# Kernel optimization log

Hardware: AMD Instinct MI355X
Metric: run time of the kernel (lower is better)

## Reference

```python
import jax, jax.numpy as jnp
import numpy as np

D = 256          # feature_dim
H = 4            # num_heads (hard-coded in AdaAttentionalPropagation)
HD = D // H      # per-head dim = 64
L = 6            # number of layers
B, N, M = 2, 2048, 2048
NAMES = ("self", "cross", "self", "cross", "self", "cross")
POOLS = (1, 1, 2, 2, 2, 2)
EPS = 1e-5


def conv1x1(W, b, x):
    # Conv1d kernel_size=1 == pointwise linear over channels: x [B, Cin, N] -> [B, Cout, N]
    return jnp.einsum('oi,bin->bon', W, x) + b[None, :, None]


def inst_norm(x):
    # InstanceNorm1d(affine=False): normalize over spatial dim per (batch, channel)
    mu = jnp.mean(x, axis=-1, keepdims=True)
    var = jnp.var(x, axis=-1, keepdims=True)
    return (x - mu) * jax.lax.rsqrt(var + EPS)


def attn_prop(params, x, source, mask):
    # One AdaAttentionalPropagation layer. x [B,D,Nq], source [B,D,Nk], mask [B,Nq,Nk]
    Wq, bq, Wk, bk, Wv, bv, Wm, bm, W1, b1, W2, b2 = params
    b = x.shape[0]
    q = conv1x1(Wq, bq, x).reshape(b, HD, H, -1)       # [B, hd, H, Nq]
    k = conv1x1(Wk, bk, source).reshape(b, HD, H, -1)  # [B, hd, H, Nk]
    v = conv1x1(Wv, bv, source).reshape(b, HD, H, -1)
    scores = jnp.einsum('bdhn,bdhm->bhnm', q, k) / np.sqrt(HD).astype(np.float32)
    scores = scores * mask[:, None]                     # multiplicative pruned mask
    prob = jax.nn.softmax(scores, axis=-1)              # [B, H, Nq, Nk]
    att = jnp.einsum('bhnm,bdhm->bdhn', prob, v).reshape(b, D, -1)
    message = conv1x1(Wm, bm, att)                      # merge
    y = jnp.concatenate([x, message], axis=1)           # [B, 2D, Nq]
    h = jax.nn.relu(inst_norm(conv1x1(W1, b1, y)))      # MLP_IN hidden
    delta = conv1x1(W2, b2, h)                          # [B, D, Nq]
    return delta, jnp.mean(prob, axis=1)                # prob averaged over heads


def prune(conn, prob, pool, k_cur):
    # update_connections_by_pooling_size: keep top (k_cur // pool) entries per row
    if prob is None or pool == 1:
        return conn, k_cur
    k_new = k_cur // pool
    vals, idxs = jax.lax.top_k(prob, k_new)             # over last axis
    b, n, _ = conn.shape
    new = jnp.zeros_like(conn).at[
        jnp.arange(b)[:, None, None], jnp.arange(n)[None, :, None], idxs
    ].set(jnp.where(vals > 0, 1.0, 0.0).astype(conn.dtype))
    return jax.lax.stop_gradient(new), k_new


def setup_inputs() -> dict:
    key = jax.random.key(0)
    ks = jax.random.split(key, 16)
    s1 = 1.0 / np.sqrt(D)
    s2 = 1.0 / np.sqrt(2 * D)
    return {
        "desc0": jax.random.normal(ks[0], (B, D, N), dtype=jnp.float32),
        "desc1": jax.random.normal(ks[1], (B, D, M), dtype=jnp.float32),
        "Wq": jax.random.normal(ks[2], (L, D, D), dtype=jnp.float32) * s1,
        "bq": jax.random.normal(ks[3], (L, D), dtype=jnp.float32) * 0.01,
        "Wk": jax.random.normal(ks[4], (L, D, D), dtype=jnp.float32) * s1,
        "bk": jax.random.normal(ks[5], (L, D), dtype=jnp.float32) * 0.01,
        "Wv": jax.random.normal(ks[6], (L, D, D), dtype=jnp.float32) * s1,
        "bv": jax.random.normal(ks[7], (L, D), dtype=jnp.float32) * 0.01,
        "Wm": jax.random.normal(ks[8], (L, D, D), dtype=jnp.float32) * s1,
        "bm": jax.random.normal(ks[9], (L, D), dtype=jnp.float32) * 0.01,
        "W1": jax.random.normal(ks[10], (L, 2 * D, 2 * D), dtype=jnp.float32) * s2,
        "b1": jax.random.normal(ks[11], (L, 2 * D), dtype=jnp.float32) * 0.01,
        "W2": jax.random.normal(ks[12], (L, D, 2 * D), dtype=jnp.float32) * s2,
        "b2": jnp.zeros((L, D), dtype=jnp.float32),  # nn.init.constant_(mlp[-1].bias, 0)
    }


def reference(desc0, desc1, Wq, bq, Wk, bk, Wv, bv, Wm, bm, W1, b1, W2, b2):
    b = desc0.shape[0]
    n, m = desc0.shape[2], desc1.shape[2]
    masks = {
        '00': jnp.ones((b, n, n), jnp.float32), '01': jnp.ones((b, n, m), jnp.float32),
        '11': jnp.ones((b, m, m), jnp.float32), '10': jnp.ones((b, m, n), jnp.float32),
    }
    probs = {'00': None, '01': None, '11': None, '10': None}
    kcnt = {'00': n, '01': m, '11': m, '10': n}
    for i in range(L):
        params = (Wq[i], bq[i], Wk[i], bk[i], Wv[i], bv[i],
                  Wm[i], bm[i], W1[i], b1[i], W2[i], b2[i])
        pool = POOLS[i]
        if NAMES[i] == 'cross':
            masks['01'], kcnt['01'] = prune(masks['01'], probs['01'], pool, kcnt['01'])
            delta0, probs['01'] = attn_prop(params, desc0, desc1, masks['01'])
            masks['10'], kcnt['10'] = prune(masks['10'], probs['10'], pool, kcnt['10'])
            delta1, probs['10'] = attn_prop(params, desc1, desc0, masks['10'])
        else:
            masks['00'], kcnt['00'] = prune(masks['00'], probs['00'], pool, kcnt['00'])
            delta0, probs['00'] = attn_prop(params, desc0, desc0, masks['00'])
            masks['11'], kcnt['11'] = prune(masks['11'], probs['11'], pool, kcnt['11'])
            delta1, probs['11'] = attn_prop(params, desc1, desc1, masks['11'])
        desc0 = desc0 + delta0
        desc1 = desc1 + delta1
    return jnp.stack([desc0, desc1])  # [2, B, D, N]
```

## Files before the change

### kernel.cpp

```cpp
#include <hip/hip_runtime.h>
#include <hip/hip_bf16.h>
#include <stdint.h>

#define NPTS 2048
#define MB_ROW 256L
#define MB_B   ((long)NPTS * MB_ROW)
#define MB_T   (2 * MB_B)

typedef __attribute__((ext_vector_type(8))) short bf16x8;
typedef __attribute__((ext_vector_type(4))) float f32x4;
#define MFMA16 __builtin_amdgcn_mfma_f32_16x16x32_bf16

__device__ inline unsigned short f2b(float f) {
  union { float f; unsigned int u; } x; x.f = f;
  unsigned int u = x.u;
  return (unsigned short)((u + 0x7FFFu + ((u >> 16) & 1u)) >> 16);
}
__device__ inline float bfu(unsigned int us) {
  union { unsigned int u; float f; } x; x.u = (us & 0xFFFFu) << 16;
  return x.f;
}
__device__ inline void sp3(float x, unsigned short& h, unsigned short& m, unsigned short& l) {
  h = f2b(x);
  float r1 = x - bfu(h);
  m = f2b(r1);
  l = f2b(r1 - bfu(m));
}
__device__ inline void gld16(const unsigned short* g, unsigned short* l) {
  __builtin_amdgcn_global_load_lds(
      (const __attribute__((address_space(1))) void*)g,
      (__attribute__((address_space(3))) void*)l, 16, 0, 0);
}

#define E_P3  0
#define E_V3  1
#define E_S3  2
#define E_Y3  3
#define E_H   4
#define E_RES 5
#define E_S3S 6

template <int EPI>
__global__ __launch_bounds__(256) void t3_k(
    const unsigned short* __restrict__ A, long aps,
    const unsigned short* __restrict__ B, long bps,
    const unsigned short* __restrict__ B2, long b2ps,
    const float* __restrict__ bias,
    void* __restrict__ out,
    const unsigned char* __restrict__ masks,
    int K, int lda, int ldb, int ksplit, long sps,
    int zbase, int xorv, int selfl, int yoff) {
  const int t = threadIdx.x;
  const int z = blockIdx.z;
  const int zg = zbase + z;
  long aoff = 0, boff = 0, b2off = 0;
  if constexpr (EPI == E_P3 || EPI == E_V3) {
    boff = (long)z * 524288;
  } else if constexpr (EPI == E_S3 || EPI == E_S3S) {
    const int sb = zg >> 2, h = zg & 3;
    aoff = (long)zg * 131072;
    boff = (long)((sb ^ xorv) * 4 + h) * 131072;
  } else if constexpr (EPI == E_Y3) {
    boff = (long)zg * 524288;
  } else if constexpr (EPI == E_H) {
    boff = (long)zg * 524288;
    b2off = (long)z * 524288;
  } else {
    boff = (long)z * 1048576;
  }
  const int n0 = blockIdx.x * 64;
  const int m0 = ((EPI == E_S3 || EPI == E_S3S) ? yoff : 0) + blockIdx.y * 64;

  __shared__ __align__(16) unsigned short As[3][64 * 64];
  __shared__ __align__(16) unsigned short Bs[3][64 * 64];
  __shared__ unsigned int Ms[128];
  if constexpr (EPI == E_S3 || EPI == E_S3S) {
    if (t < 128) {
      const int sb = zg >> 2;
      const int type = selfl ? (sb >> 1) : 2 + (sb >> 1);
      const unsigned int* mw =
          (const unsigned int*)(masks + (long)type * MB_T + (long)(sb & 1) * MB_B);
      Ms[t] = mw[(long)(m0 + (t >> 1)) * 64 + (n0 >> 5) + (t & 1)];
    }
  }

  const int w = t >> 6;
  const int L = t & 63;
  const int wm = (w & 1) * 32, wn = (w >> 1) * 32;
  const int lr = t & 15, lk = (t >> 4) & 3;
  const int swr = (lr & 7) << 3;
  const int grow = (L >> 3);
  const int gj = L & 7;

  f32x4 acc[2][2];
#pragma unroll
  for (int i = 0; i < 2; ++i)
#pragma unroll
    for (int j = 0; j < 2; ++j) acc[i][j] = (f32x4){0.f, 0.f, 0.f, 0.f};

  for (int k0 = 0; k0 < K; k0 += 64) {
    const unsigned short* Bsel;
    long bo, bp;
    int kb;
    if (k0 < ksplit) { Bsel = B; bo = boff; bp = bps; kb = k0; }
    else             { Bsel = B2; bo = b2off; bp = b2ps; kb = k0 - ksplit; }
    if (k0) __syncthreads();
#pragma unroll
    for (int pl = 0; pl < 3; ++pl) {
      const unsigned short* Ap = A + (long)pl * aps + aoff;
      const unsigned short* Bp = Bsel + (long)pl * bp + bo;
#pragma unroll
      for (int c = 0; c < 2; ++c) {
        const int rbase = w * 16 + c * 8;
        const int row = rbase + grow;
        const int colA = (gj ^ (row & 7)) << 3;
        gld16(&Ap[(long)(m0 + row) * lda + k0 + colA], &As[pl][rbase * 64]);
        gld16(&Bp[(long)(n0 + row) * ldb + kb + colA], &Bs[pl][rbase * 64]);
      }
    }
    __syncthreads();
#pragma unroll
    for (int kk = 0; kk < 2; ++kk) {
      bf16x8 af[3][2], bf[3][2];
#pragma unroll
      for (int pl = 0; pl < 3; ++pl)
#pragma unroll
        for (int mi = 0; mi < 2; ++mi) {
          af[pl][mi] = *(const bf16x8*)&As[pl][(wm + mi * 16 + lr) * 64 + ((kk * 32 + lk * 8) ^ swr)];
          bf[pl][mi] = *(const bf16x8*)&Bs[pl][(wn + mi * 16 + lr) * 64 + ((kk * 32 + lk * 8) ^ swr)];
        }
#pragma unroll
      for (int mi = 0; mi < 2; ++mi)
#pragma unroll
        for (int ni = 0; ni < 2; ++ni) {
          f32x4 c = acc[mi][ni];
          c = MFMA16(af[2][mi], bf[0][ni], c, 0, 0, 0);
          c = MFMA16(af[0][mi], bf[2][ni], c, 0, 0, 0);
          c = MFMA16(af[1][mi], bf[1][ni], c, 0, 0, 0);
          c = MFMA16(af[1][mi], bf[0][ni], c, 0, 0, 0);
          c = MFMA16(af[0][mi], bf[1][ni], c, 0, 0, 0);
          c = MFMA16(af[0][mi], bf[0][ni], c, 0, 0, 0);
          acc[mi][ni] = c;
        }
    }
  }

  if constexpr (EPI == E_S3 || EPI == E_S3S) {
    __syncthreads();
    float* ST = (float*)&As[0][0];
#pragma unroll
    for (int mi = 0; mi < 2; ++mi)
#pragma unroll
      for (int ni = 0; ni < 2; ++ni)
#pragma unroll
        for (int r = 0; r < 4; ++r)
          ST[(wm + mi * 16 + lk * 4 + r) * 68 + wn + ni * 16 + lr] = acc[mi][ni][r];
    __syncthreads();
    float* o = (float*)out;
#pragma unroll
    for (int it = 0; it < 4; ++it) {
      const int row = (t >> 4) + it * 16;
      const int col = (t & 15) * 4;
      float4 vv = *(const float4*)&ST[row * 68 + col];
      const unsigned int mw = Ms[row * 2 + (col >> 5)];
      vv.x = ((mw >> ((col + 0) & 31)) & 1u) ? vv.x * 0.125f : 0.f;
      vv.y = ((mw >> ((col + 1) & 31)) & 1u) ? vv.y * 0.125f : 0.f;
      vv.z = ((mw >> ((col + 2) & 31)) & 1u) ? vv.z * 0.125f : 0.f;
      vv.w = ((mw >> ((col + 3) & 31)) & 1u) ? vv.w * 0.125f : 0.f;
      const int rloc = blockIdx.y * 64 + row;
      *(float4*)&o[(long)z * sps + (long)rloc * 2048 + n0 + col] = vv;
      if constexpr (EPI == E_S3S) {
        float2* pst = (float2*)const_cast<float*>(bias);
        const int CHrows = (int)(sps >> 11);
        float mx4 = fmaxf(fmaxf(vv.x, vv.y), fmaxf(vv.z, vv.w));
#pragma unroll
        for (int oo = 1; oo < 16; oo <<= 1) mx4 = fmaxf(mx4, __shfl_xor(mx4, oo));
        float e4 = __expf(vv.x - mx4) + __expf(vv.y - mx4) +
                   __expf(vv.z - mx4) + __expf(vv.w - mx4);
#pragma unroll
        for (int oo = 1; oo < 16; oo <<= 1) e4 += __shfl_xor(e4, oo);
        if ((t & 15) == 0)
          pst[((long)z * CHrows + rloc) * 32 + blockIdx.x] = make_float2(mx4, e4);
      }
    }
    return;
  }

#pragma unroll
  for (int mi = 0; mi < 2; ++mi) {
#pragma unroll
    for (int ni = 0; ni < 2; ++ni) {
      f32x4 a = acc[mi][ni];
      const int cM = m0 + wm + mi * 16 + lk * 4;
      const int pN = n0 + wn + ni * 16 + lr;
      if constexpr (EPI == E_P3) {
        float4 bv4 = *(const float4*)&bias[cM];
        float bb[4] = {bv4.x, bv4.y, bv4.z, bv4.w};
        unsigned short* o = (unsigned short*)out;
        const long b0 = (long)z * 524288 + (long)pN * 64 + (cM >> 2);
#pragma unroll
        for (int r = 0; r < 4; ++r) {
          unsigned short h_, m_, l_;
          sp3(a[r] + bb[r], h_, m_, l_);
          const long ad = b0 + (long)r * 131072;
          o[ad] = h_; o[ad + 2097152] = m_; o[ad + 4194304] = l_;
        }
      } else if constexpr (EPI == E_V3) {
        float4 bv4 = *(const float4*)&bias[cM];
        float bb[4] = {bv4.x, bv4.y, bv4.z, bv4.w};
        unsigned short* o = (unsigned short*)out;
        const long b0 = (long)z * 524288 + (long)(cM >> 2) * 2048 + pN;
#pragma unroll
        for (int r = 0; r < 4; ++r) {
          unsigned short h_, m_, l_;
          sp3(a[r] + bb[r], h_, m_, l_);
          const long ad = b0 + (long)r * 131072;
          o[ad] = h_; o[ad + 2097152] = m_; o[ad + 4194304] = l_;
        }
      } else if constexpr (EPI == E_Y3) {
        float4 bv4 = *(const float4*)&bias[cM];
        float bb[4] = {bv4.x, bv4.y, bv4.z, bv4.w};
        unsigned short* o = (unsigned short*)out;
        ushort4 h4, m4, l4;
        unsigned short* hp = (unsigned short*)&h4;
        unsigned short* mp = (unsigned short*)&m4;
        unsigned short* lp = (unsigned short*)&l4;
#pragma unroll
        for (int r = 0; r < 4; ++r) sp3(a[r] + bb[r], hp[r], mp[r], lp[r]);
        const long b0 = (long)z * 524288 + (long)pN * 256 + cM;
        *(ushort4*)&o[b0] = h4;
        *(ushort4*)&o[b0 + sps] = m4;
        *(ushort4*)&o[b0 + 2 * sps] = l4;
      } else if constexpr (EPI == E_H) {
        *(f32x4*)&((float*)out)[(long)z * 1048576 + (long)pN * 512 + cM] = a;
      } else {
        float4 bv4 = *(const float4*)&bias[cM];
        float* p = &((float*)out)[(long)zg * 524288 + (long)pN * 256 + cM];
        float4 old = *(const float4*)p;
        float4 nw;
        nw.x = old.x + a[0] + bv4.x; nw.y = old.y + a[1] + bv4.y;
        nw.z = old.z + a[2] + bv4.z; nw.w = old.w + a[3] + bv4.w;
        *(float4*)p = nw;
      }
    }
  }
}

__global__ __launch_bounds__(256) void stat_k(const float2* __restrict__ pst,
                                              float2* __restrict__ stats) {
  const int idx = blockIdx.x * 256 + threadIdx.x;
  const float2* p = pst + (long)idx * 32;
  float m = p[0].x;
#pragma unroll
  for (int i = 1; i < 32; ++i) m = fmaxf(m, p[i].x);
  float s = 0.f;
#pragma unroll
  for (int i = 0; i < 32; ++i) s += p[i].y * __expf(p[i].x - m);
  stats[idx] = make_float2(m, 1.0f / s);
}

__global__ __launch_bounds__(256) void softmax_prune_k(
    const float* __restrict__ S, float2* __restrict__ stats,
    unsigned char* __restrict__ masks,
    int knew, int sbG, int cb, int selfl, long sps, int CH) {
  const int lane = threadIdx.x & 63;
  const int wv = threadIdx.x >> 6;
  const int nl = blockIdx.x * 4 + wv;

  __shared__ float meanL[4 * 32 * 64];
  __shared__ int hist[4 * 256];
  float* myMean = &meanL[(wv * 32) * 64 + lane];

#pragma unroll
  for (int j = 0; j < 32; ++j) myMean[j * 64] = 0.f;

  float mx4[4], ri4[4];
#pragma unroll
  for (int hh = 0; hh < 4; ++hh) {
    const float* row = S + (long)hh * sps + (long)nl * 2048 + lane * 32;
    float xs[32];
#pragma unroll
    for (int e = 0; e < 8; ++e) {
      float4 u = *(const float4*)(row + e * 4);
      xs[e * 4 + 0] = u.x; xs[e * 4 + 1] = u.y;
      xs[e * 4 + 2] = u.z; xs[e * 4 + 3] = u.w;
    }
    float m = xs[0];
#pragma unroll
    for (int j = 1; j < 32; ++j) m = fmaxf(m, xs[j]);
    for (int o = 32; o; o >>= 1) m = fmaxf(m, __shfl_xor(m, o));
    float s = 0.f;
#pragma unroll
    for (int j = 0; j < 32; ++j) { xs[j] = __expf(xs[j] - m); s += xs[j]; }
    for (int o = 32; o; o >>= 1) s += __shfl_xor(s, o);
    const float ri = 1.0f / s;
    mx4[hh] = m; ri4[hh] = ri;
#pragma unroll
    for (int j = 0; j < 32; ++j)
      myMean[j * 64] += 0.25f * (xs[j] * ri);
  }
  if (lane == 0) {
#pragma unroll
    for (int hh = 0; hh < 4; ++hh)
      stats[(long)hh * CH + nl] = make_float2(mx4[hh], ri4[hh]);
  }

  unsigned int key[32];
#pragma unroll
  for (int j = 0; j < 32; ++j) key[j] = __float_as_uint(myMean[j * 64]);

  int* hw = &hist[wv * 256];
  unsigned int pref = 0;
  int kneed = knew;
  for (int pass = 0; pass < 4; ++pass) {
    const int shift = 24 - pass * 8;
    const unsigned int hm = (pass == 0) ? 0u : (0xFFFFFFFFu << (shift + 8));
#pragma unroll
    for (int b = 0; b < 4; ++b) hw[b * 64 + lane] = 0;
    __syncthreads();
#pragma unroll
    for (int j = 0; j < 32; ++j)
      if ((key[j] & hm) == pref) atomicAdd(&hw[(key[j] >> shift) & 255], 1);
    __syncthreads();
    int own[4];
    int tot = 0;
#pragma unroll
    for (int e = 0; e < 4; ++e) { own[e] = hw[lane * 4 + e]; tot += own[e]; }
    int suf = tot;
    for (int o = 1; o < 64; o <<= 1) {
      int tmp = __shfl_down(suf, o);
      if (lane + o < 64) suf += tmp;
    }
    int run = suf - tot;
    int pack = 0;
#pragma unroll
    for (int e = 3; e >= 0; --e) {
      const int Sb = run + own[e];
      if (Sb >= kneed && run < kneed) pack = ((lane * 4 + e) << 20) | (run + 1);
      run = Sb;
    }
    for (int o = 1; o < 64; o <<= 1) pack |= __shfl_xor(pack, o);
    const int bin = pack >> 20;
    const int above = (pack & 0xFFFFF) - 1;
    pref |= ((unsigned int)bin) << shift;
    kneed -= above;
  }
  const unsigned int T = pref;
  const int take = kneed;
  int cnt = 0;
#pragma unroll
  for (int j = 0; j < 32; ++j) cnt += (key[j] == T);
  int pc = cnt;
  for (int o = 1; o < 64; o <<= 1) {
    int tmp = __shfl_up(pc, o);
    if (lane >= o) pc += tmp;
  }
  int base = pc - cnt;
  uchar4 ob;
  unsigned char* obp = (unsigned char*)&ob;
#pragma unroll
  for (int byte = 0; byte < 4; ++byte) {
    unsigned int bb = 0;
#pragma unroll
    for (int e = 0; e < 8; ++e) {
      const int j = byte * 8 + e;
      int sel = 0;
      if (key[j] > T) sel = 1;
      else if (key[j] == T) { if (T > 0u && base < take) sel = 1; base++; }
      bb |= (unsigned int)sel << e;
    }
    obp[byte] = (unsigned char)bb;
  }
  const int type = selfl ? (sbG >> 1) : 2 + (sbG >> 1);
  unsigned char* mb = masks + (long)type * MB_T + (long)(sbG & 1) * MB_B;
  *(uchar4*)&mb[(long)(cb + nl) * MB_ROW + lane * 4] = ob;
}

__global__ __launch_bounds__(256) void pv3_k(
    const unsigned short* __restrict__ V3, const float* __restrict__ S, long sps,
    const float2* __restrict__ stats, int CH,
    float* __restrict__ part, int zbase, int xorv) {
  const int t = threadIdx.x;
  const int h = blockIdx.z;
  const int kseg = blockIdx.y;
  const int n0 = blockIdx.x * 64;
  const int sb = zbase >> 2;
  const unsigned short* Vb = V3 + (long)((sb ^ xorv) * 4 + h) * 131072;
  const float* Sp = S + (long)h * sps;
  const float2* sth = stats + (long)h * CH;

  __shared__ __align__(16) unsigned short Bs[3][64 * 64];

  const int w = t >> 6;
  const int wm = (w & 1) * 32, wn = (w >> 1) * 32;
  const int lr = t & 15, lk = (t >> 4) & 3;
  const int srow = t >> 3, scol = (t & 7) * 8;
  const int sws = scol ^ ((srow & 7) << 3);
  const int swr = (lr & 7) << 3;

  f32x4 acc[2][2];
#pragma unroll
  for (int i = 0; i < 2; ++i)
#pragma unroll
    for (int j = 0; j < 2; ++j) acc[i][j] = (f32x4){0.f, 0.f, 0.f, 0.f};

  const int kbeg = kseg * 256;
  const float2 st0 = sth[n0 + srow];
  const float2 st1 = sth[n0 + 32 + srow];
  const float* srcA = &Sp[(long)(n0 + srow) * 2048 + kbeg + scol];
  const float* srcB = &Sp[(long)(n0 + 32 + srow) * 2048 + kbeg + scol];

  float4 c0a = *(const float4*)srcA;
  float4 c0b = *(const float4*)(srcA + 4);
  float4 c1a = *(const float4*)srcB;
  float4 c1b = *(const float4*)(srcB + 4);

#pragma unroll
  for (int ki = 0; ki < 4; ++ki) {
    const int k0 = kbeg + ki * 64;
    float4 n0a, n0b, n1a, n1b;
    if (ki < 3) {
      const int off = (ki + 1) * 64;
      n0a = *(const float4*)(srcA + off);
      n0b = *(const float4*)(srcA + off + 4);
      n1a = *(const float4*)(srcB + off);
      n1b = *(const float4*)(srcB + off + 4);
    }
    if (ki) __syncthreads();
    {
      float xs[8] = {c0a.x, c0a.y, c0a.z, c0a.w, c0b.x, c0b.y, c0b.z, c0b.w};
      ushort4 hq[2], mq[2], lq[2];
      unsigned short* hp = (unsigned short*)hq;
      unsigned short* mp = (unsigned short*)mq;
      unsigned short* lp = (unsigned short*)lq;
#pragma unroll
      for (int j = 0; j < 8; ++j) {
        float p = __expf(xs[j] - st0.x) * st0.y;
        sp3(p, hp[j], mp[j], lp[j]);
      }
      *(ushort4*)&Bs[0][srow * 64 + sws] = hq[0];
      *(ushort4*)&Bs[0][srow * 64 + sws + 4] = hq[1];
      *(ushort4*)&Bs[1][srow * 64 + sws] = mq[0];
      *(ushort4*)&Bs[1][srow * 64 + sws + 4] = mq[1];
      *(ushort4*)&Bs[2][srow * 64 + sws] = lq[0];
      *(ushort4*)&Bs[2][srow * 64 + sws + 4] = lq[1];
    }
    {
      float xs[8] = {c1a.x, c1a.y, c1a.z, c1a.w, c1b.x, c1b.y, c1b.z, c1b.w};
      ushort4 hq[2], mq[2], lq[2];
      unsigned short* hp = (unsigned short*)hq;
      unsigned short* mp = (unsigned short*)mq;
      unsigned short* lp = (unsigned short*)lq;
#pragma unroll
      for (int j = 0; j < 8; ++j) {
        float p = __expf(xs[j] - st1.x) * st1.y;
        sp3(p, hp[j], mp[j], lp[j]);
      }
      const int rr = 32 + srow;
      *(ushort4*)&Bs[0][rr * 64 + sws] = hq[0];
      *(ushort4*)&Bs[0][rr * 64 + sws + 4] = hq[1];
      *(ushort4*)&Bs[1][rr * 64 + sws] = mq[0];
      *(ushort4*)&Bs[1][rr * 64 + sws + 4] = mq[1];
      *(ushort4*)&Bs[2][rr * 64 + sws] = lq[0];
      *(ushort4*)&Bs[2][rr * 64 + sws + 4] = lq[1];
    }
    __syncthreads();
#pragma unroll
    for (int kk = 0; kk < 2; ++kk) {
      bf16x8 af[3][2], bf[3][2];
#pragma unroll
      for (int pl = 0; pl < 3; ++pl) {
#pragma unroll
        for (int mi = 0; mi < 2; ++mi) {
          af[pl][mi] = *(const bf16x8*)&Vb[(long)pl * 2097152 +
                                           (long)(wm + mi * 16 + lr) * 2048 + k0 + kk * 32 + lk * 8];
          bf[pl][mi] = *(const bf16x8*)&Bs[pl][(wn + mi * 16 + lr) * 64 + ((kk * 32 + lk * 8) ^ swr)];
        }
      }
#pragma unroll
      for (int mi = 0; mi < 2; ++mi)
#pragma unroll
        for (int ni = 0; ni < 2; ++ni) {
          f32x4 c = acc[mi][ni];
          c = MFMA16(af[2][mi], bf[0][ni], c, 0, 0, 0);
          c = MFMA16(af[0][mi], bf[2][ni], c, 0, 0, 0);
          c = MFMA16(af[1][mi], bf[1][ni], c, 0, 0, 0);
          c = MFMA16(af[1][mi], bf[0][ni], c, 0, 0, 0);
          c = MFMA16(af[0][mi], bf[1][ni], c, 0, 0, 0);
          c = MFMA16(af[0][mi], bf[0][ni], c, 0, 0, 0);
          acc[mi][ni] = c;
        }
    }
    if (ki < 3) { c0a = n0a; c0b = n0b; c1a = n1a; c1b = n1b; }
  }

  float* pp = part + (((long)kseg * 4 + h) * CH) * 64;
#pragma unroll
  for (int mi = 0; mi < 2; ++mi) {
#pragma unroll
    for (int ni = 0; ni < 2; ++ni) {
      const int cM = wm + mi * 16 + lk * 4;
      const int pN = n0 + wn + ni * 16 + lr;
      *(f32x4*)&pp[(long)pN * 64 + cM] = acc[mi][ni];
    }
  }
}

__global__ __launch_bounds__(256) void comb_k(const float* __restrict__ part,
                                              unsigned short* __restrict__ att3,
                                              int CH, int sb, int cb) {
  const int q = threadIdx.x & 63;
  const int g = threadIdx.x >> 6;
  const int nl = blockIdx.x * 4 + g;
  float s[4] = {0.f, 0.f, 0.f, 0.f};
#pragma unroll
  for (int ks = 0; ks < 8; ++ks)
#pragma unroll
    for (int h = 0; h < 4; ++h)
      s[h] += part[(((long)ks * 4 + h) * CH + nl) * 64 + q];
  ushort4 h4, m4, l4;
  unsigned short* hp = (unsigned short*)&h4;
  unsigned short* mp = (unsigned short*)&m4;
  unsigned short* lp = (unsigned short*)&l4;
#pragma unroll
  for (int h = 0; h < 4; ++h) sp3(s[h], hp[h], mp[h], lp[h]);
  const long base = (long)sb * 524288 + (long)(cb + nl) * 256 + 4 * q;
  *(ushort4*)&att3[base] = h4;
  *(ushort4*)&att3[base + 2097152] = m4;
  *(ushort4*)&att3[base + 4194304] = l4;
}

__global__ __launch_bounds__(256) void inormA_k(const float* __restrict__ H,
                                                float* __restrict__ partial) {
  const int seg = blockIdx.x, sbl = blockIdx.y;
  const float* hp = H + (long)sbl * 1048576;
  const int t = threadIdx.x;
  float s0 = 0.f, q0 = 0.f, s1 = 0.f, q1 = 0.f;
  const int r0 = seg * 64;
  for (int r = r0; r < r0 + 64; ++r) {
    float x0 = hp[(long)r * 512 + t];
    float x1 = hp[(long)r * 512 + t + 256];
    s0 += x0; q0 = fmaf(x0, x0, q0);
    s1 += x1; q1 = fmaf(x1, x1, q1);
  }
  float* pp = partial + ((long)sbl * 32 + seg) * 1024;
  pp[t] = s0; pp[t + 256] = s1;
  pp[512 + t] = q0; pp[512 + t + 256] = q1;
}

__global__ __launch_bounds__(256) void inormB_k(const float* __restrict__ partial,
                                                float* __restrict__ stats2) {
  const int sbl = blockIdx.x;
  const int t = threadIdx.x;
  const float* pp = partial + (long)sbl * 32768;
  float a0 = 0.f, b0 = 0.f, a1 = 0.f, b1 = 0.f;
  for (int seg = 0; seg < 32; ++seg) {
    const float* p = pp + seg * 1024;
    a0 += p[t]; a1 += p[t + 256];
    b0 += p[512 + t]; b1 += p[512 + t + 256];
  }
  float mu0 = a0 * (1.f / 2048.f);
  float mu1 = a1 * (1.f / 2048.f);
  float rs0 = rsqrtf(b0 * (1.f / 2048.f) - mu0 * mu0 + 1e-5f);
  float rs1 = rsqrtf(b1 * (1.f / 2048.f) - mu1 * mu1 + 1e-5f);
  float* st = stats2 + (long)sbl * 1024;
  st[t] = mu0; st[t + 256] = mu1;
  st[512 + t] = rs0; st[512 + t + 256] = rs1;
}

__global__ __launch_bounds__(256) void inormC_k(const float* __restrict__ H,
                                                const float* __restrict__ stats2,
                                                unsigned short* __restrict__ HB,
                                                long hps) {
  const int seg = blockIdx.x, sbl = blockIdx.y;
  const float* hp = H + (long)sbl * 1048576;
  unsigned short* hb = HB + (long)sbl * 1048576;
  const float* st = stats2 + (long)sbl * 1024;
  const int t = threadIdx.x;
  const float mu0 = st[t], mu1 = st[t + 256];
  const float rs0 = st[512 + t], rs1 = st[512 + t + 256];
  const int r0 = seg * 64;
  for (int r = r0; r < r0 + 64; ++r) {
    float x0 = hp[(long)r * 512 + t];
    float x1 = hp[(long)r * 512 + t + 256];
    float o0 = (x0 - mu0) * rs0; o0 = o0 > 0.f ? o0 : 0.f;
    float o1 = (x1 - mu1) * rs1; o1 = o1 > 0.f ? o1 : 0.f;
    unsigned short h_, m_, l_;
    sp3(o0, h_, m_, l_);
    const long ad0 = (long)r * 512 + t;
    hb[ad0] = h_; hb[ad0 + hps] = m_; hb[ad0 + 2 * hps] = l_;
    sp3(o1, h_, m_, l_);
    const long ad1 = ad0 + 256;
    hb[ad1] = h_; hb[ad1 + hps] = m_; hb[ad1 + 2 * hps] = l_;
  }
}

__global__ __launch_bounds__(256) void split6_k(
    const float* __restrict__ q, const float* __restrict__ k,
    const float* __restrict__ v, const float* __restrict__ m,
    const float* __restrict__ w1, const float* __restrict__ w2,
    unsigned short* __restrict__ dst) {
  long i = ((long)blockIdx.x * 256 + threadIdx.x) * 4;
  const float* src;
  long off, base, ps;
  if (i < 262144) {
    int sel = (int)(i >> 16);
    src = sel == 0 ? q : sel == 1 ? k : sel == 2 ? v : m;
    off = i & 65535; base = (long)sel * 196608; ps = 65536;
  } else if (i < 524288) {
    src = w1; off = i - 262144; base = 786432; ps = 262144;
  } else {
    src = w2; off = i - 524288; base = 1572864; ps = 131072;
  }
  float4 vv = *(const float4*)&src[off];
  float xs[4] = {vv.x, vv.y, vv.z, vv.w};
  ushort4 h4, m4, l4;
  unsigned short* hp = (unsigned short*)&h4;
  unsigned short* mp = (unsigned short*)&m4;
  unsigned short* lp = (unsigned short*)&l4;
#pragma unroll
  for (int j = 0; j < 4; ++j) sp3(xs[j], hp[j], mp[j], lp[j]);
  *(ushort4*)&dst[base + off] = h4;
  *(ushort4*)&dst[base + ps + off] = m4;
  *(ushort4*)&dst[base + 2 * ps + off] = l4;
}

__global__ __launch_bounds__(256) void split3_k(const float* __restrict__ src,
                                                unsigned short* __restrict__ dst,
                                                long plane, long n) {
  long i = ((long)blockIdx.x * 256 + threadIdx.x) * 4;
  if (i >= n) return;
  float4 v = *(const float4*)&src[i];
  float xs[4] = {v.x, v.y, v.z, v.w};
  ushort4 h4, m4, l4;
  unsigned short* hp = (unsigned short*)&h4;
  unsigned short* mp = (unsigned short*)&m4;
  unsigned short* lp = (unsigned short*)&l4;
#pragma unroll
  for (int j = 0; j < 4; ++j) sp3(xs[j], hp[j], mp[j], lp[j]);
  *(ushort4*)&dst[i] = h4;
  *(ushort4*)&dst[plane + i] = m4;
  *(ushort4*)&dst[2 * plane + i] = l4;
}

__global__ __launch_bounds__(256) void tin_k(const float* __restrict__ d0,
                                             const float* __restrict__ d1,
                                             float* __restrict__ descT) {
  __shared__ float tl[32][33];
  const int sb = blockIdx.z, s = sb >> 1, b = sb & 1;
  const float* src = (s ? d1 : d0) + (long)b * 524288;
  const int p0 = blockIdx.x * 32, c0 = blockIdx.y * 32;
  const int tx = threadIdx.x & 31, ty = threadIdx.x >> 5;
#pragma unroll
  for (int i = 0; i < 4; ++i)
    tl[ty + i * 8][tx] = src[(long)(c0 + ty + i * 8) * 2048 + p0 + tx];
  __syncthreads();
#pragma unroll
  for (int i = 0; i < 4; ++i)
    descT[(long)sb * 524288 + (long)(p0 + ty + i * 8) * 256 + c0 + tx] = tl[tx][ty + i * 8];
}

__global__ __launch_bounds__(256) void tout_k(const float* __restrict__ descT,
                                              float* __restrict__ out) {
  __shared__ float tl[32][33];
  const int sb = blockIdx.z;
  const int p0 = blockIdx.x * 32, c0 = blockIdx.y * 32;
  const int tx = threadIdx.x & 31, ty = threadIdx.x >> 5;
#pragma unroll
  for (int i = 0; i < 4; ++i)
    tl[ty + i * 8][tx] = descT[(long)sb * 524288 + (long)(p0 + ty + i * 8) * 256 + c0 + tx];
  __syncthreads();
#pragma unroll
  for (int i = 0; i < 4; ++i)
    out[(long)sb * 524288 + (long)(c0 + ty + i * 8) * 2048 + p0 + tx] = tl[tx][ty + i * 8];
}

extern "C" void kernel_launch(void* const* d_in, const int* in_sizes, int n_in,
                              void* d_out, int out_size, void* d_ws, size_t ws_size,
                              hipStream_t stream) {
  (void)in_sizes; (void)n_in; (void)out_size;
  const float* in_d0 = (const float*)d_in[0];
  const float* in_d1 = (const float*)d_in[1];
  const float* Wq = (const float*)d_in[2];
  const float* bq = (const float*)d_in[3];
  const float* Wk = (const float*)d_in[4];
  const float* bk = (const float*)d_in[5];
  const float* Wv = (const float*)d_in[6];
  const float* bv = (const float*)d_in[7];
  const float* Wm = (const float*)d_in[8];
  const float* bm = (const float*)d_in[9];
  const float* W1 = (const float*)d_in[10];
  const float* b1 = (const float*)d_in[11];
  const float* W2 = (const float*)d_in[12];
  const float* b2 = (const float*)d_in[13];
  (void)b1;

  const long region_b = (long)ws_size - 79429632;
  const int CH = (region_b >= 40992L * 2048) ? 2048
               : (region_b >= 40992L * 1024) ? 1024 : 512;
  const int nchunks = 2048 / CH;
  const long sps = (long)CH * 2048;
  const int mb = (region_b >= 4 * 13766656L) ? 4 : (region_b >= 2 * 13766656L) ? 2 : 1;

  uint8_t* w = (uint8_t*)d_ws;
  float* descT          = (float*)w;
  unsigned short* desc3 = (unsigned short*)(w + 8388608);
  unsigned short* Q3    = (unsigned short*)(w + 20971520);
  unsigned short* K3    = (unsigned short*)(w + 33554432);
  unsigned short* V3    = (unsigned short*)(w + 46137344);
  unsigned short* att3  = (unsigned short*)(w + 58720256);
  unsigned short* wbuf  = (unsigned short*)(w + 71303168);
  unsigned char* masks  = w + 75235328;
  uint8_t* region       = w + 79429632;
  float* S              = (float*)region;
  float* part           = (float*)(region + (long)CH * 32768);
  float2* pst           = (float2*)part;
  float2* stats         = (float2*)(region + (long)CH * 32768 + (long)CH * 8192);
  unsigned short* msg3  = (unsigned short*)region;
  float* hbuf           = (float*)(region + (long)mb * 3145728);
  unsigned short* hB3   = (unsigned short*)(region + (long)mb * 7340032);
  float* inpart         = (float*)(region + (long)mb * 13631488);
  float* instats        = (float*)(region + (long)mb * 13631488 + (long)mb * 131072);

  const unsigned short* wq3 = wbuf;
  const unsigned short* wk3 = wbuf + 196608;
  const unsigned short* wv3 = wbuf + 393216;
  const unsigned short* wm3 = wbuf + 589824;
  const unsigned short* w13 = wbuf + 786432;
  const unsigned short* w23 = wbuf + 1572864;

  tin_k<<<dim3(64, 8, 4), 256, 0, stream>>>(in_d0, in_d1, descT);
  hipMemsetAsync(masks, 0xFF, 4 * MB_T, stream);

  for (int l = 0; l < 6; ++l) {
    const int selfl = (l % 2 == 0);
    const int xorv = selfl ? 0 : 2;
    const int knew = (l < 2) ? 1024 : (l < 4) ? 512 : 0;

    split6_k<<<dim3(640), 256, 0, stream>>>(Wq + (long)l * 65536, Wk + (long)l * 65536,
                                            Wv + (long)l * 65536, Wm + (long)l * 65536,
                                            W1 + (long)l * 262144, W2 + (long)l * 131072,
                                            wbuf);
    split3_k<<<dim3(2048), 256, 0, stream>>>(descT, desc3, 2097152, 2097152);

    t3_k<E_P3><<<dim3(32, 4, 4), 256, 0, stream>>>(
        wq3, 65536, desc3, 2097152, nullptr, 0, bq + l * 256, Q3, nullptr,
        256, 256, 256, 1 << 30, 0, 0, 0, 0, 0);
    t3_k<E_P3><<<dim3(32, 4, 4), 256, 0, stream>>>(
        wk3, 65536, desc3, 2097152, nullptr, 0, bk + l * 256, K3, nullptr,
        256, 256, 256, 1 << 30, 0, 0, 0, 0, 0);
    t3_k<E_V3><<<dim3(32, 4, 4), 256, 0, stream>>>(
        wv3, 65536, desc3, 2097152, nullptr, 0, bv + l * 256, V3, nullptr,
        256, 256, 256, 1 << 30, 0, 0, 0, 0, 0);

    for (int sb = 0; sb < 4; ++sb) {
      for (int c = 0; c < nchunks; ++c) {
        const int cb = c * CH;
        if (knew) {
          t3_k<E_S3><<<dim3(32, CH / 64, 4), 256, 0, stream>>>(
              Q3, 2097152, K3, 2097152, nullptr, 0, nullptr, S, masks,
              64, 64, 64, 1 << 30, sps, sb * 4, xorv, selfl, cb);
          softmax_prune_k<<<dim3(CH / 4), 256, 0, stream>>>(
              S, stats, masks, knew, sb, cb, selfl, sps, CH);
        } else {
          t3_k<E_S3S><<<dim3(32, CH / 64, 4), 256, 0, stream>>>(
              Q3, 2097152, K3, 2097152, nullptr, 0, (const float*)pst, S, masks,
              64, 64, 64, 1 << 30, sps, sb * 4, xorv, selfl, cb);
          stat_k<<<dim3(4 * CH / 256), 256, 0, stream>>>(pst, stats);
        }
        pv3_k<<<dim3(CH / 64, 8, 4), 256, 0, stream>>>(V3, S, sps, stats, CH, part, sb * 4, xorv);
        comb_k<<<dim3(CH / 4), 256, 0, stream>>>(part, att3, CH, sb, cb);
      }
    }

    for (int p = 0; p < 4; p += mb) {
      t3_k<E_Y3><<<dim3(32, 4, mb), 256, 0, stream>>>(
          wm3, 65536, att3, 2097152, nullptr, 0, bm + l * 256, msg3, nullptr,
          256, 256, 256, 1 << 30, (long)mb * 524288, p, 0, 0, 0);
      t3_k<E_H><<<dim3(32, 8, mb), 256, 0, stream>>>(
          w13, 262144, desc3, 2097152, msg3, (long)mb * 524288, nullptr, hbuf, nullptr,
          512, 512, 256, 256, 0, p, 0, 0, 0);
      inormA_k<<<dim3(32, mb), 256, 0, stream>>>(hbuf, inpart);
      inormB_k<<<dim3(mb), 256, 0, stream>>>(inpart, instats);
      inormC_k<<<dim3(32, mb), 256, 0, stream>>>(hbuf, instats, hB3, (long)mb * 1048576);
      t3_k<E_RES><<<dim3(32, 4, mb), 256, 0, stream>>>(
          w23, 131072, hB3, (long)mb * 1048576, nullptr, 0, b2 + l * 256, descT, nullptr,
          512, 512, 512, 1 << 30, 0, p, 0, 0, 0);
    }
  }

  tout_k<<<dim3(64, 8, 4), 256, 0, stream>>>(descT, (float*)d_out);
}
```

Measured before the change: 2.870 ms.

## Parallelize softmax-prune per row across four waves with block-wide radix select

The softmax/top-k pruning kernel now gives each row a whole 256-thread block instead of one wave, so each wave computes one head's softmax. The head-averaged probabilities are combined through swizzled shared memory. The radix select uses a single block-wide histogram with cross-wave suffix sums. This raises parallelism fourfold (CH blocks instead of CH/4) and cuts per-thread register and LDS footprint, in exchange for more __syncthreads barriers per radix pass.

```diff
diff --git a/kernel.cpp b/kernel.cpp
--- a/kernel.cpp
+++ b/kernel.cpp
@@ -31,6 +31,7 @@
       (const __attribute__((address_space(1))) void*)g,
       (__attribute__((address_space(3))) void*)l, 16, 0, 0);
 }
+__device__ inline int swzF(int F) { return F ^ ((F >> 3) & 7); }
 
 #define E_P3  0
 #define E_V3  1
@@ -263,21 +264,18 @@
     const float* __restrict__ S, float2* __restrict__ stats,
     unsigned char* __restrict__ masks,
     int knew, int sbG, int cb, int selfl, long sps, int CH) {
-  const int lane = threadIdx.x & 63;
-  const int wv = threadIdx.x >> 6;
-  const int nl = blockIdx.x * 4 + wv;
-
-  __shared__ float meanL[4 * 32 * 64];
-  __shared__ int hist[4 * 256];
-  float* myMean = &meanL[(wv * 32) * 64 + lane];
-
-#pragma unroll
-  for (int j = 0; j < 32; ++j) myMean[j * 64] = 0.f;
-
-  float mx4[4], ri4[4];
-#pragma unroll
-  for (int hh = 0; hh < 4; ++hh) {
-    const float* row = S + (long)hh * sps + (long)nl * 2048 + lane * 32;
+  const int t = threadIdx.x;
+  const int lane = t & 63;
+  const int wv = t >> 6;
+  const int nl = blockIdx.x;
+
+  __shared__ __align__(16) float4 pL4[4][512];
+  __shared__ int hist[256];
+  __shared__ int wred[4];
+  __shared__ int sbx[2];
+
+  {
+    const float* row = S + (long)wv * sps + (long)nl * 2048 + lane * 32;
     float xs[32];
 #pragma unroll
     for (int e = 0; e < 8; ++e) {
@@ -294,86 +292,102 @@
     for (int j = 0; j < 32; ++j) { xs[j] = __expf(xs[j] - m); s += xs[j]; }
     for (int o = 32; o; o >>= 1) s += __shfl_xor(s, o);
     const float ri = 1.0f / s;
-    mx4[hh] = m; ri4[hh] = ri;
-#pragma unroll
-    for (int j = 0; j < 32; ++j)
-      myMean[j * 64] += 0.25f * (xs[j] * ri);
-  }
-  if (lane == 0) {
-#pragma unroll
-    for (int hh = 0; hh < 4; ++hh)
-      stats[(long)hh * CH + nl] = make_float2(mx4[hh], ri4[hh]);
-  }
-
-  unsigned int key[32];
-#pragma unroll
-  for (int j = 0; j < 32; ++j) key[j] = __float_as_uint(myMean[j * 64]);
-
-  int* hw = &hist[wv * 256];
+    if (lane == 0) stats[(long)wv * CH + nl] = make_float2(m, ri);
+#pragma unroll
+    for (int e = 0; e < 8; ++e) {
+      float4 pv;
+      pv.x = xs[e * 4 + 0] * ri; pv.y = xs[e * 4 + 1] * ri;
+      pv.z = xs[e * 4 + 2] * ri; pv.w = xs[e * 4 + 3] * ri;
+      pL4[wv][swzF(lane * 8 + e)] = pv;
+    }
+  }
+  __syncthreads();
+
+  unsigned int key[8];
+  {
+#pragma unroll
+    for (int jj = 0; jj < 2; ++jj) {
+      const int Fs = swzF(t * 2 + jj);
+      float4 p0 = pL4[0][Fs];
+      float4 p1 = pL4[1][Fs];
+      float4 p2 = pL4[2][Fs];
+      float4 p3 = pL4[3][Fs];
+      float4 mm;
+      mm.x = 0.25f * p0.x; mm.x += 0.25f * p1.x; mm.x += 0.25f * p2.x; mm.x += 0.25f * p3.x;
+      mm.y = 0.25f * p0.y; mm.y += 0.25f * p1.y; mm.y += 0.25f * p2.y; mm.y += 0.25f * p3.y;
+      mm.z = 0.25f * p0.z; mm.z += 0.25f * p1.z; mm.z += 0.25f * p2.z; mm.z += 0.25f * p3.z;
+      mm.w = 0.25f * p0.w; mm.w += 0.25f * p1.w; mm.w += 0.25f * p2.w; mm.w += 0.25f * p3.w;
+      key[jj * 4 + 0] = __float_as_uint(mm.x);
+      key[jj * 4 + 1] = __float_as_uint(mm.y);
+      key[jj * 4 + 2] = __float_as_uint(mm.z);
+      key[jj * 4 + 3] = __float_as_uint(mm.w);
+    }
+  }
+
   unsigned int pref = 0;
   int kneed = knew;
   for (int pass = 0; pass < 4; ++pass) {
     const int shift = 24 - pass * 8;
+    hist[t] = 0;
+    __syncthreads();
     const unsigned int hm = (pass == 0) ? 0u : (0xFFFFFFFFu << (shift + 8));
 #pragma unroll
-    for (int b = 0; b < 4; ++b) hw[b * 64 + lane] = 0;
+    for (int j = 0; j < 8; ++j) {
+      unsigned int k = key[j];
+      if ((k & hm) == pref) atomicAdd(&hist[(k >> shift) & 255], 1);
+    }
     __syncthreads();
-#pragma unroll
-    for (int j = 0; j < 32; ++j)
-      if ((key[j] & hm) == pref) atomicAdd(&hw[(key[j] >> shift) & 255], 1);
+    const int h = hist[t];
+    int s = h;
+#pragma unroll
+    for (int o = 1; o < 64; o <<= 1) {
+      int tmp = __shfl_down(s, o);
+      if (lane + o < 64) s += tmp;
+    }
+    if (lane == 0) wred[wv] = s;
     __syncthreads();
-    int own[4];
-    int tot = 0;
-#pragma unroll
-    for (int e = 0; e < 4; ++e) { own[e] = hw[lane * 4 + e]; tot += own[e]; }
-    int suf = tot;
-    for (int o = 1; o < 64; o <<= 1) {
-      int tmp = __shfl_down(suf, o);
-      if (lane + o < 64) suf += tmp;
-    }
-    int run = suf - tot;
-    int pack = 0;
-#pragma unroll
-    for (int e = 3; e >= 0; --e) {
-      const int Sb = run + own[e];
-      if (Sb >= kneed && run < kneed) pack = ((lane * 4 + e) << 20) | (run + 1);
-      run = Sb;
-    }
-    for (int o = 1; o < 64; o <<= 1) pack |= __shfl_xor(pack, o);
-    const int bin = pack >> 20;
-    const int above = (pack & 0xFFFFF) - 1;
-    pref |= ((unsigned int)bin) << shift;
-    kneed -= above;
+    int addhi = 0;
+#pragma unroll
+    for (int w2 = 0; w2 < 4; ++w2)
+      if (w2 > wv) addhi += wred[w2];
+    s += addhi;
+    const int above = s - h;
+    if (s >= kneed && above < kneed) { sbx[0] = t; sbx[1] = above; }
+    __syncthreads();
+    pref |= ((unsigned int)sbx[0]) << shift;
+    kneed -= sbx[1];
+    __syncthreads();
   }
   const unsigned int T = pref;
   const int take = kneed;
   int cnt = 0;
 #pragma unroll
-  for (int j = 0; j < 32; ++j) cnt += (key[j] == T);
+  for (int j = 0; j < 8; ++j) cnt += (key[j] == T);
   int pc = cnt;
+#pragma unroll
   for (int o = 1; o < 64; o <<= 1) {
     int tmp = __shfl_up(pc, o);
     if (lane >= o) pc += tmp;
   }
-  int base = pc - cnt;
-  uchar4 ob;
-  unsigned char* obp = (unsigned char*)&ob;
-#pragma unroll
-  for (int byte = 0; byte < 4; ++byte) {
-    unsigned int bb = 0;
-#pragma unroll
-    for (int e = 0; e < 8; ++e) {
-      const int j = byte * 8 + e;
-      int sel = 0;
-      if (key[j] > T) sel = 1;
-      else if (key[j] == T) { if (T > 0u && base < take) sel = 1; base++; }
-      bb |= (unsigned int)sel << e;
-    }
-    obp[byte] = (unsigned char)bb;
+  if (lane == 63) wred[wv] = pc;
+  __syncthreads();
+  int woff = 0;
+#pragma unroll
+  for (int w2 = 0; w2 < 4; ++w2)
+    if (w2 < wv) woff += wred[w2];
+  int base = woff + pc - cnt;
+  unsigned int byte = 0;
+#pragma unroll
+  for (int j = 0; j < 8; ++j) {
+    unsigned int k = key[j];
+    int sel = 0;
+    if (k > T) sel = 1;
+    else if (k == T) { if (T > 0u && base < take) sel = 1; base++; }
+    byte |= (unsigned int)sel << j;
   }
   const int type = selfl ? (sbG >> 1) : 2 + (sbG >> 1);
   unsigned char* mb = masks + (long)type * MB_T + (long)(sbG & 1) * MB_B;
-  *(uchar4*)&mb[(long)(cb + nl) * MB_ROW + lane * 4] = ob;
+  mb[(long)(cb + nl) * MB_ROW + t] = (unsigned char)byte;
 }
 
 __global__ __launch_bounds__(256) void pv3_k(
@@ -760,7 +774,7 @@
           t3_k<E_S3><<<dim3(32, CH / 64, 4), 256, 0, stream>>>(
               Q3, 2097152, K3, 2097152, nullptr, 0, nullptr, S, masks,
               64, 64, 64, 1 << 30, sps, sb * 4, xorv, selfl, cb);
-          softmax_prune_k<<<dim3(CH / 4), 256, 0, stream>>>(
+          softmax_prune_k<<<dim3(CH), 256, 0, stream>>>(
               S, stats, masks, knew, sb, cb, selfl, sps, CH);
         } else {
           t3_k<E_S3S><<<dim3(32, CH / 64, 4), 256, 0, stream>>>(
```

Result: no change. 2.834 ms (median of 2 runs) (-1.2%).
